# Optimization experiments

Measured on AMD Instinct MI355X. Metric: run time of the kernel, lower is better.

Reference implementation:

```python
import jax, jax.numpy as jnp
import numpy as np

B, N, F_IN, F_OUT, H = 8, 1024, 128, 128, 8
NEG_SLOPE = 0.2


def setup_inputs() -> dict:
    key = jax.random.key(0)
    k1, k2, k3, k4, k5 = jax.random.split(key, 5)
    h = jax.random.normal(k1, (B, N, F_IN), dtype=jnp.float32)
    adj = jax.random.randint(k2, (N, N), 0, 2, dtype=jnp.int32)
    bias_matrix = jax.random.normal(k3, (1, 1, N, N), dtype=jnp.float32)
    # Xavier-uniform-ish parameter init matching torch Parameter shapes
    limW = float(np.sqrt(6.0 / (F_IN + F_OUT)))
    W = jax.random.uniform(k4, (H, F_IN, F_OUT), minval=-limW, maxval=limW, dtype=jnp.float32)
    lima = float(np.sqrt(6.0 / (2 * F_OUT + 1)))
    a = jax.random.uniform(k5, (H, 2 * F_OUT, 1), minval=-lima, maxval=lima, dtype=jnp.float32)
    return {"h": h, "adj": adj, "bias_matrix": bias_matrix, "W": W, "a": a}


def reference(h, adj, bias_matrix, W, a):
    # h: [B,N,Fin], adj: [N,N] int, bias_matrix: [1,1,N,N]
    Fo = W.shape[-1]
    h_prime = jnp.einsum('bni,hio->bnho', h, W)  # [B,N,H,Fo]
    # e[b,i,j,h] = leakyrelu(cat(hp_i, hp_j) . a_h) = leakyrelu(hp_i.a1 + hp_j.a2)
    a1 = a[:, :Fo, 0]   # [H,Fo]
    a2 = a[:, Fo:, 0]   # [H,Fo]
    s_i = jnp.einsum('bnhf,hf->bnh', h_prime, a1)  # [B,N,H]
    s_j = jnp.einsum('bnhf,hf->bnh', h_prime, a2)  # [B,N,H]
    e = jax.nn.leaky_relu(s_i[:, :, None, :] + s_j[:, None, :, :], NEG_SLOPE)  # [B,N,N,H]
    # bias: [1,1,N,N] -> expand(B,1,N,N) -> permute -> [B,N,N,1] -> broadcast H
    e = e + bias_matrix[0, 0][None, :, :, None]
    mask = (adj != 0)[None, :, :, None]  # [1,N,N,1]
    e = jnp.where(mask, e, -jnp.inf)
    attention = jax.nn.softmax(e, axis=2)  # softmax over source nodes j
    h_out = jnp.einsum('bijh,bjhf->bihf', attention, h_prime)  # [B,N,H,Fo]
    # concat=False -> mean over heads
    return h_out.mean(axis=2)  # [B,N,Fo]
```

## Files before the change

kernel.cpp:

```cpp
#include <hip/hip_runtime.h>
#include <hip/hip_bf16.h>
#include <math.h>

#define B_   8
#define N_   1024
#define FIN  128
#define FOUT 128
#define H_   8
#define NEG  0.2f
#define LOG2E 1.4426950408889634f

typedef __attribute__((ext_vector_type(4))) float f32x4;
typedef __attribute__((ext_vector_type(8))) short s16x8;

static __device__ __forceinline__ unsigned short f2bf(float f) {
    unsigned int u = __float_as_uint(f);
    unsigned int r = (u + 0x7fffu + ((u >> 16) & 1u)) >> 16;
    return (unsigned short)r;
}

static __device__ __forceinline__ unsigned short f2bf_hw(float f) {
    union { __hip_bfloat16 b; unsigned short u; } cv;
    cv.b = __float2bfloat16(f);
    return cv.u;
}

__global__ __launch_bounds__(256) void k_prep(const int* __restrict__ adj,
                                              const float* __restrict__ bias,
                                              const float* __restrict__ W,
                                              const float* __restrict__ a,
                                              const float* __restrict__ hsrc,
                                              float* __restrict__ biasm,
                                              unsigned short* __restrict__ WT,
                                              float* __restrict__ wa,
                                              unsigned short* __restrict__ hbT,
                                              float* __restrict__ outz) {
    __shared__ float tf[64][132];
    const int blk = blockIdx.x;
    const int t   = threadIdx.x;

    if (blk < 1024) {
        const int base = (blk * 256 + t) * 4;
        int4   av = *(const int4*)&adj[base];
        float4 bv = *(const float4*)&bias[base];
        const float NINF = -__builtin_inff();
        float4 r;
        r.x = av.x ? bv.x * LOG2E : NINF;
        r.y = av.y ? bv.y * LOG2E : NINF;
        r.z = av.z ? bv.z * LOG2E : NINF;
        r.w = av.w ? bv.w * LOG2E : NINF;
        *(float4*)&biasm[base] = r;
    } else if (blk < 1032) {
        const int hd  = blk - 1024;
        const int fo  = t >> 1;
        const int fi0 = (t & 1) * 64;
        const float* src = W + (size_t)hd * FIN * FOUT;
        unsigned short* dst = WT + ((size_t)hd * FOUT + fo) * FIN + fi0;
#pragma unroll
        for (int c = 0; c < 8; ++c) {
            s16x8 v;
#pragma unroll
            for (int u = 0; u < 8; ++u)
                v[u] = (short)f2bf(src[(size_t)(fi0 + c * 8 + u) * FOUT + fo]);
            *(s16x8*)(dst + c * 8) = v;
        }
    } else if (blk < 1040) {
        const int hd = blk - 1032;
        const int which = t >> 7, k = t & 127;
        const float* wrow = W + ((size_t)hd * FIN + k) * FOUT;
        const float* av   = a + (size_t)hd * 2 * FOUT + which * FOUT;
        float s = 0.f;
#pragma unroll 8
        for (int f = 0; f < FOUT; f += 4) {
            float4 wv = *(const float4*)&wrow[f];
            float4 a4 = *(const float4*)&av[f];
            s += wv.x * a4.x + wv.y * a4.y + wv.z * a4.z + wv.w * a4.w;
        }
        wa[((size_t)hd * 2 + which) * FIN + k] = s * LOG2E;
    } else if (blk < 1168) {
        const int bn0 = (blk - 1040) * 64;
        const int b   = bn0 >> 10;
        const int n0  = bn0 & 1023;
        {
            const int r = t >> 2, k0 = (t & 3) * 32;
            const float* src = hsrc + (size_t)(bn0 + r) * FIN + k0;
#pragma unroll
            for (int c = 0; c < 8; ++c)
                *(float4*)&tf[r][k0 + c * 4] = *(const float4*)&src[c * 4];
        }
        __syncthreads();
        {
            const int k   = t >> 1;
            const int seg = (t & 1) * 32;
            unsigned short* dst = hbT + ((size_t)b * FIN + k) * N_ + n0 + seg;
#pragma unroll
            for (int c = 0; c < 4; ++c) {
                s16x8 v;
#pragma unroll
                for (int u = 0; u < 8; ++u)
                    v[u] = (short)f2bf_hw(tf[seg + c * 8 + u][k]);
                *(s16x8*)(dst + c * 8) = v;
            }
        }
    } else {
        const int base = ((blk - 1168) * 256 + t) * 8;
        const float4 z4 = make_float4(0.f, 0.f, 0.f, 0.f);
        *(float4*)&outz[base]     = z4;
        *(float4*)&outz[base + 4] = z4;
    }
}

__global__ __launch_bounds__(256) void k_s12(const float* __restrict__ hsrc,
                                             const float* __restrict__ wa,
                                             float* __restrict__ s1,
                                             float* __restrict__ s2T) {
    __shared__ float hrow[16][132];
    __shared__ float wal[16][132];
    const int t   = threadIdx.x;
    const int bn0 = blockIdx.x * 16;
    {
        const int r = t >> 4, c = (t & 15) * 8;
        *(float4*)&wal[r][c]     = *(const float4*)&wa[r * FIN + c];
        *(float4*)&wal[r][c + 4] = *(const float4*)&wa[r * FIN + c + 4];
        *(float4*)&hrow[r][c]     = *(const float4*)&hsrc[(size_t)(bn0 + r) * FIN + c];
        *(float4*)&hrow[r][c + 4] = *(const float4*)&hsrc[(size_t)(bn0 + r) * FIN + c + 4];
    }
    __syncthreads();
    const int r = t >> 4, sub = t & 15;
    const int hd = sub >> 1, which = sub & 1;
    float s = 0.f;
#pragma unroll 8
    for (int k = 0; k < FIN; k += 4) {
        float4 hv = *(const float4*)&hrow[r][k];
        float4 wv = *(const float4*)&wal[sub][k];
        s += hv.x * wv.x + hv.y * wv.y + hv.z * wv.z + hv.w * wv.w;
    }
    const int bn = bn0 + r;
    if (which == 0) s1[(size_t)bn * 8 + hd] = s;
    else            s2T[(size_t)hd * (B_ * N_) + bn] = s;
}

__global__ __launch_bounds__(256, 5) void k_pv2(const unsigned short* __restrict__ hbT,
                                                const float* __restrict__ s1,
                                                const float* __restrict__ s2T,
                                                const float* __restrict__ biasm,
                                                const unsigned short* __restrict__ WT,
                                                float* __restrict__ out) {
    __shared__ __align__(16) unsigned short P[32][72];
    __shared__ __align__(16) unsigned short Bl[128 * 64];
    __shared__ __align__(16) unsigned short Gl[32][136];
    __shared__ float Zl[32];
    const int t    = threadIdx.x;
    const int lane = t & 63;
    const int wave = t >> 6;
    const int wg  = blockIdx.x;
    const int swz = ((wg & 7) << 8) | (wg >> 3);
    const int i0  = (swz & 31) * 32;
    const int hd  = (swz >> 5) & 7;
    const int b   = swz >> 8;

    const int prow = t >> 3;
    const int pj0  = (t & 7) * 8;
    const int gi   = (b << 10) + i0 + prow;
    const float s1v = s1[(size_t)gi * 8 + hd];
    const float* bm_row = biasm + (size_t)(i0 + prow) * N_;
    const float* s2p    = s2T + (size_t)hd * (B_ * N_) + (b << 10);

    const unsigned short* hpS = hbT + (size_t)b * FIN * N_;
    const int brow = t >> 3;
    const int bc   = t & 7;

    const int wr = (wave & 1) * 16;
    const int wc = (wave >> 1) * 64;
    const int arow = wr + (lane & 15);
    const int koff = (lane >> 4) * 8;

    f32x4 acc[4];
#pragma unroll
    for (int j = 0; j < 4; ++j) acc[j] = (f32x4){0.f, 0.f, 0.f, 0.f};
    float z_acc = 0.f;

    float4 bmv[2], sv[2];
    s16x8 Breg[4];

    auto load_it = [&](int j0) {
#pragma unroll
        for (int q = 0; q < 2; ++q) {
            bmv[q] = *(const float4*)&bm_row[j0 + pj0 + q * 4];
            sv[q]  = *(const float4*)&s2p[j0 + pj0 + q * 4];
        }
    };
    auto bload = [&](int j0) {
#pragma unroll
        for (int q = 0; q < 4; ++q)
            Breg[q] = *(const s16x8*)&hpS[(size_t)(brow + q * 32) * N_ + j0 + bc * 8];
    };
    auto phaseA = [&]() {
#pragma unroll
        for (int q = 0; q < 4; ++q) {
            int row = brow + q * 32;
            *(s16x8*)&Bl[row * 64 + ((bc ^ (row & 7)) * 8)] = Breg[q];
        }
        s16x8 pv;
#pragma unroll
        for (int q = 0; q < 2; ++q) {
            float x0 = s1v + sv[q].x; x0 = fmaxf(x0, NEG * x0) + bmv[q].x;
            float x1 = s1v + sv[q].y; x1 = fmaxf(x1, NEG * x1) + bmv[q].y;
            float x2 = s1v + sv[q].z; x2 = fmaxf(x2, NEG * x2) + bmv[q].z;
            float x3 = s1v + sv[q].w; x3 = fmaxf(x3, NEG * x3) + bmv[q].w;
            float p0 = exp2f(x0);
            float p1 = exp2f(x1);
            float p2 = exp2f(x2);
            float p3 = exp2f(x3);
            z_acc += (p0 + p1) + (p2 + p3);
            pv[q * 4 + 0] = (short)f2bf_hw(p0);
            pv[q * 4 + 1] = (short)f2bf_hw(p1);
            pv[q * 4 + 2] = (short)f2bf_hw(p2);
            pv[q * 4 + 3] = (short)f2bf_hw(p3);
        }
        *(s16x8*)&P[prow][pj0] = pv;
    };

    bload(0);
    load_it(0);
    for (int it = 0; it < 16; ++it) {
        const int j0 = it * 64;
        phaseA();
        __syncthreads();
        if (it < 15) { bload(j0 + 64); load_it(j0 + 64); }
#pragma unroll
        for (int kw = 0; kw < 2; ++kw) {
            s16x8 a0 = *(const s16x8*)&P[arow][kw * 32 + koff];
#pragma unroll
            for (int fc = 0; fc < 4; ++fc) {
                const int r = wc + fc * 16 + (lane & 15);
                const int chunk = (lane >> 4) + kw * 4;
                s16x8 bf = *(const s16x8*)&Bl[r * 64 + ((chunk ^ (r & 7)) * 8)];
                acc[fc] = __builtin_amdgcn_mfma_f32_16x16x32_bf16(a0, bf, acc[fc], 0, 0, 0);
            }
        }
        __syncthreads();
    }

    float z = z_acc;
    z += __shfl_xor(z, 1); z += __shfl_xor(z, 2); z += __shfl_xor(z, 4);
    if ((t & 7) == 0) Zl[prow] = 0.125f / z;

    const unsigned short* Wsrc = WT + (size_t)hd * FOUT * FIN;
    s16x8 Wreg[4];
#pragma unroll
    for (int q = 0; q < 4; ++q)
        Wreg[q] = *(const s16x8*)&Wsrc[(size_t)(brow + q * 32) * FIN + bc * 8];
    __syncthreads();

#pragma unroll
    for (int r = 0; r < 4; ++r) {
        const int il = wr + (lane >> 4) * 4 + r;
        const float sc = Zl[il];
#pragma unroll
        for (int fc = 0; fc < 4; ++fc)
            Gl[il][wc + fc * 16 + (lane & 15)] = f2bf_hw(acc[fc][r] * sc);
    }
#pragma unroll
    for (int q = 0; q < 4; ++q) {
        int row = brow + q * 32;
        *(s16x8*)&Bl[row * 64 + ((bc ^ (row & 7)) * 8)] = Wreg[q];
    }
#pragma unroll
    for (int q = 0; q < 4; ++q)
        Wreg[q] = *(const s16x8*)&Wsrc[(size_t)(brow + q * 32) * FIN + 64 + bc * 8];
    __syncthreads();

    const int wr2 = (wave & 1) * 16;
    const int wc2 = (wave >> 1) * 64;
    f32x4 acc2[4];
#pragma unroll
    for (int j = 0; j < 4; ++j) acc2[j] = (f32x4){0.f, 0.f, 0.f, 0.f};

#pragma unroll
    for (int kw = 0; kw < 2; ++kw) {
        s16x8 a0 = *(const s16x8*)&Gl[wr2 + (lane & 15)][kw * 32 + koff];
#pragma unroll
        for (int fc = 0; fc < 4; ++fc) {
            const int rb = wc2 + fc * 16 + (lane & 15);
            const int chunk = (lane >> 4) + kw * 4;
            s16x8 bf = *(const s16x8*)&Bl[rb * 64 + ((chunk ^ (rb & 7)) * 8)];
            acc2[fc] = __builtin_amdgcn_mfma_f32_16x16x32_bf16(a0, bf, acc2[fc], 0, 0, 0);
        }
    }
    __syncthreads();
#pragma unroll
    for (int q = 0; q < 4; ++q) {
        int row = brow + q * 32;
        *(s16x8*)&Bl[row * 64 + ((bc ^ (row & 7)) * 8)] = Wreg[q];
    }
    __syncthreads();
#pragma unroll
    for (int kw = 0; kw < 2; ++kw) {
        s16x8 a0 = *(const s16x8*)&Gl[wr2 + (lane & 15)][64 + kw * 32 + koff];
#pragma unroll
        for (int fc = 0; fc < 4; ++fc) {
            const int rb = wc2 + fc * 16 + (lane & 15);
            const int chunk = (lane >> 4) + kw * 4;
            s16x8 bf = *(const s16x8*)&Bl[rb * 64 + ((chunk ^ (rb & 7)) * 8)];
            acc2[fc] = __builtin_amdgcn_mfma_f32_16x16x32_bf16(a0, bf, acc2[fc], 0, 0, 0);
        }
    }

#pragma unroll
    for (int r = 0; r < 4; ++r) {
        const int il = wr2 + (lane >> 4) * 4 + r;
        float* op = out + ((size_t)((b << 10) + i0 + il)) * FOUT + wc2 + (lane & 15);
#pragma unroll
        for (int fc = 0; fc < 4; ++fc)
            unsafeAtomicAdd(op + fc * 16, acc2[fc][r]);
    }
}

extern "C" void kernel_launch(void* const* d_in, const int* in_sizes, int n_in,
                              void* d_out, int out_size, void* d_ws, size_t ws_size,
                              hipStream_t stream) {
    const float* hsrc = (const float*)d_in[0];
    const int*   adj  = (const int*)d_in[1];
    const float* bias = (const float*)d_in[2];
    const float* W    = (const float*)d_in[3];
    const float* a    = (const float*)d_in[4];
    float* out = (float*)d_out;

    char* ws = (char*)d_ws;
    unsigned short* hbT = (unsigned short*)ws;
    float* s1    = (float*)(ws + 2097152);
    float* s2T   = s1 + 65536;
    float* biasm = s2T + 65536;
    unsigned short* WT = (unsigned short*)(biasm + N_ * N_);
    float* wa = (float*)(WT + (size_t)H_ * FOUT * FIN);

    k_prep<<<dim3(1680), 256, 0, stream>>>(adj, bias, W, a, hsrc,
                                           biasm, WT, wa, hbT, out);
    k_s12<<<dim3(B_ * N_ / 16), 256, 0, stream>>>(hsrc, wa, s1, s2T);
    k_pv2<<<dim3(2048), 256, 0, stream>>>(hbT, s1, s2T, biasm, WT, out);
}
```

Before: 76.29 us.

## Process two heads per workgroup to reuse staged h tiles, swizzle P, move zeroing

Each k_pv2 workgroup now handles two attention heads, so the bf16 h tile staged in shared memory is loaded once and feeds two sets of MFMAs. This halves the grid and halves the global traffic for h and the bias matrix. The P buffer is doubled and gets an XOR swizzle to avoid LDS bank conflicts, and output zeroing moves from k_prep into k_s12. The cost is more accumulator registers, so the occupancy hint drops from 5 to 4, and the per-block epilogue does twice the W projection work serially.

```diff
diff --git a/kernel.cpp b/kernel.cpp
--- a/kernel.cpp
+++ b/kernel.cpp
@@ -33,8 +33,7 @@
                                               float* __restrict__ biasm,
                                               unsigned short* __restrict__ WT,
                                               float* __restrict__ wa,
-                                              unsigned short* __restrict__ hbT,
-                                              float* __restrict__ outz) {
+                                              unsigned short* __restrict__ hbT) {
     __shared__ float tf[64][132];
     const int blk = blockIdx.x;
     const int t   = threadIdx.x;
@@ -77,7 +76,7 @@
             s += wv.x * a4.x + wv.y * a4.y + wv.z * a4.z + wv.w * a4.w;
         }
         wa[((size_t)hd * 2 + which) * FIN + k] = s * LOG2E;
-    } else if (blk < 1168) {
+    } else {
         const int bn0 = (blk - 1040) * 64;
         const int b   = bn0 >> 10;
         const int n0  = bn0 & 1023;
@@ -102,22 +101,26 @@
                 *(s16x8*)(dst + c * 8) = v;
             }
         }
-    } else {
-        const int base = ((blk - 1168) * 256 + t) * 8;
+    }
+}
+
+__global__ __launch_bounds__(256) void k_s12(const float* __restrict__ hsrc,
+                                             const float* __restrict__ wa,
+                                             float* __restrict__ s1,
+                                             float* __restrict__ s2T,
+                                             float* __restrict__ outz) {
+    __shared__ float hrow[16][132];
+    __shared__ float wal[16][132];
+    const int t   = threadIdx.x;
+    const int blk = blockIdx.x;
+    if (blk >= 512) {
+        const int base = ((blk - 512) * 256 + t) * 8;
         const float4 z4 = make_float4(0.f, 0.f, 0.f, 0.f);
         *(float4*)&outz[base]     = z4;
         *(float4*)&outz[base + 4] = z4;
-    }
-}
-
-__global__ __launch_bounds__(256) void k_s12(const float* __restrict__ hsrc,
-                                             const float* __restrict__ wa,
-                                             float* __restrict__ s1,
-                                             float* __restrict__ s2T) {
-    __shared__ float hrow[16][132];
-    __shared__ float wal[16][132];
-    const int t   = threadIdx.x;
-    const int bn0 = blockIdx.x * 16;
+        return;
+    }
+    const int bn0 = blk * 16;
     {
         const int r = t >> 4, c = (t & 15) * 8;
         *(float4*)&wal[r][c]     = *(const float4*)&wa[r * FIN + c];
@@ -140,31 +143,35 @@
     else            s2T[(size_t)hd * (B_ * N_) + bn] = s;
 }
 
-__global__ __launch_bounds__(256, 5) void k_pv2(const unsigned short* __restrict__ hbT,
+__global__ __launch_bounds__(256, 4) void k_pv2(const unsigned short* __restrict__ hbT,
                                                 const float* __restrict__ s1,
                                                 const float* __restrict__ s2T,
                                                 const float* __restrict__ biasm,
                                                 const unsigned short* __restrict__ WT,
                                                 float* __restrict__ out) {
-    __shared__ __align__(16) unsigned short P[32][72];
+    __shared__ __align__(16) unsigned short P[2][32 * 64];
     __shared__ __align__(16) unsigned short Bl[128 * 64];
     __shared__ __align__(16) unsigned short Gl[32][136];
-    __shared__ float Zl[32];
+    __shared__ float Zl[2][32];
     const int t    = threadIdx.x;
     const int lane = t & 63;
     const int wave = t >> 6;
     const int wg  = blockIdx.x;
-    const int swz = ((wg & 7) << 8) | (wg >> 3);
+    const int swz = ((wg & 7) << 7) | (wg >> 3);
     const int i0  = (swz & 31) * 32;
-    const int hd  = (swz >> 5) & 7;
-    const int b   = swz >> 8;
+    const int hp  = (swz >> 5) & 3;
+    const int b   = swz >> 7;
+    const int hd0 = hp * 2, hd1 = hd0 + 1;
 
     const int prow = t >> 3;
     const int pj0  = (t & 7) * 8;
+    const int pchk = (t & 7) ^ (prow & 7);
     const int gi   = (b << 10) + i0 + prow;
-    const float s1v = s1[(size_t)gi * 8 + hd];
+    const float s1v0 = s1[(size_t)gi * 8 + hd0];
+    const float s1v1 = s1[(size_t)gi * 8 + hd1];
     const float* bm_row = biasm + (size_t)(i0 + prow) * N_;
-    const float* s2p    = s2T + (size_t)hd * (B_ * N_) + (b << 10);
+    const float* s2p0   = s2T + (size_t)hd0 * (B_ * N_) + (b << 10);
+    const float* s2p1   = s2T + (size_t)hd1 * (B_ * N_) + (b << 10);
 
     const unsigned short* hpS = hbT + (size_t)b * FIN * N_;
     const int brow = t >> 3;
@@ -175,19 +182,23 @@
     const int arow = wr + (lane & 15);
     const int koff = (lane >> 4) * 8;
 
-    f32x4 acc[4];
-#pragma unroll
-    for (int j = 0; j < 4; ++j) acc[j] = (f32x4){0.f, 0.f, 0.f, 0.f};
-    float z_acc = 0.f;
-
-    float4 bmv[2], sv[2];
+    f32x4 acc0[4], acc1[4];
+#pragma unroll
+    for (int j = 0; j < 4; ++j) {
+        acc0[j] = (f32x4){0.f, 0.f, 0.f, 0.f};
+        acc1[j] = (f32x4){0.f, 0.f, 0.f, 0.f};
+    }
+    float z0 = 0.f, z1 = 0.f;
+
+    float4 bmv[2], sv0[2], sv1[2];
     s16x8 Breg[4];
 
     auto load_it = [&](int j0) {
 #pragma unroll
         for (int q = 0; q < 2; ++q) {
             bmv[q] = *(const float4*)&bm_row[j0 + pj0 + q * 4];
-            sv[q]  = *(const float4*)&s2p[j0 + pj0 + q * 4];
+            sv0[q] = *(const float4*)&s2p0[j0 + pj0 + q * 4];
+            sv1[q] = *(const float4*)&s2p1[j0 + pj0 + q * 4];
         }
     };
     auto bload = [&](int j0) {
@@ -195,30 +206,34 @@
         for (int q = 0; q < 4; ++q)
             Breg[q] = *(const s16x8*)&hpS[(size_t)(brow + q * 32) * N_ + j0 + bc * 8];
     };
-    auto phaseA = [&]() {
-#pragma unroll
-        for (int q = 0; q < 4; ++q) {
-            int row = brow + q * 32;
-            *(s16x8*)&Bl[row * 64 + ((bc ^ (row & 7)) * 8)] = Breg[q];
-        }
+    auto pgen = [&](int h, float s1v, const float4* svh, float& zr) {
         s16x8 pv;
 #pragma unroll
         for (int q = 0; q < 2; ++q) {
-            float x0 = s1v + sv[q].x; x0 = fmaxf(x0, NEG * x0) + bmv[q].x;
-            float x1 = s1v + sv[q].y; x1 = fmaxf(x1, NEG * x1) + bmv[q].y;
-            float x2 = s1v + sv[q].z; x2 = fmaxf(x2, NEG * x2) + bmv[q].z;
-            float x3 = s1v + sv[q].w; x3 = fmaxf(x3, NEG * x3) + bmv[q].w;
+            float x0 = s1v + svh[q].x; x0 = fmaxf(x0, NEG * x0) + bmv[q].x;
+            float x1 = s1v + svh[q].y; x1 = fmaxf(x1, NEG * x1) + bmv[q].y;
+            float x2 = s1v + svh[q].z; x2 = fmaxf(x2, NEG * x2) + bmv[q].z;
+            float x3 = s1v + svh[q].w; x3 = fmaxf(x3, NEG * x3) + bmv[q].w;
             float p0 = exp2f(x0);
             float p1 = exp2f(x1);
             float p2 = exp2f(x2);
             float p3 = exp2f(x3);
-            z_acc += (p0 + p1) + (p2 + p3);
+            zr += (p0 + p1) + (p2 + p3);
             pv[q * 4 + 0] = (short)f2bf_hw(p0);
             pv[q * 4 + 1] = (short)f2bf_hw(p1);
             pv[q * 4 + 2] = (short)f2bf_hw(p2);
             pv[q * 4 + 3] = (short)f2bf_hw(p3);
         }
-        *(s16x8*)&P[prow][pj0] = pv;
+        *(s16x8*)&P[h][prow * 64 + pchk * 8] = pv;
+    };
+    auto phaseA = [&]() {
+#pragma unroll
+        for (int q = 0; q < 4; ++q) {
+            int row = brow + q * 32;
+            *(s16x8*)&Bl[row * 64 + ((bc ^ (row & 7)) * 8)] = Breg[q];
+        }
+        pgen(0, s1v0, sv0, z0);
+        pgen(1, s1v1, sv1, z1);
     };
 
     bload(0);
@@ -230,45 +245,37 @@
         if (it < 15) { bload(j0 + 64); load_it(j0 + 64); }
 #pragma unroll
         for (int kw = 0; kw < 2; ++kw) {
-            s16x8 a0 = *(const s16x8*)&P[arow][kw * 32 + koff];
+            const int chunk = kw * 4 + (lane >> 4);
+            const int aoff = (chunk ^ (arow & 7)) * 8;
+            s16x8 a00 = *(const s16x8*)&P[0][arow * 64 + aoff];
+            s16x8 a01 = *(const s16x8*)&P[1][arow * 64 + aoff];
 #pragma unroll
             for (int fc = 0; fc < 4; ++fc) {
                 const int r = wc + fc * 16 + (lane & 15);
-                const int chunk = (lane >> 4) + kw * 4;
                 s16x8 bf = *(const s16x8*)&Bl[r * 64 + ((chunk ^ (r & 7)) * 8)];
-                acc[fc] = __builtin_amdgcn_mfma_f32_16x16x32_bf16(a0, bf, acc[fc], 0, 0, 0);
+                acc0[fc] = __builtin_amdgcn_mfma_f32_16x16x32_bf16(a00, bf, acc0[fc], 0, 0, 0);
+                acc1[fc] = __builtin_amdgcn_mfma_f32_16x16x32_bf16(a01, bf, acc1[fc], 0, 0, 0);
             }
         }
         __syncthreads();
     }
 
-    float z = z_acc;
-    z += __shfl_xor(z, 1); z += __shfl_xor(z, 2); z += __shfl_xor(z, 4);
-    if ((t & 7) == 0) Zl[prow] = 0.125f / z;
-
-    const unsigned short* Wsrc = WT + (size_t)hd * FOUT * FIN;
+    {
+        float za = z0, zb = z1;
+        za += __shfl_xor(za, 1); za += __shfl_xor(za, 2); za += __shfl_xor(za, 4);
+        zb += __shfl_xor(zb, 1); zb += __shfl_xor(zb, 2); zb += __shfl_xor(zb, 4);
+        if ((t & 7) == 0) {
+            Zl[0][prow] = 0.125f / za;
+            Zl[1][prow] = 0.125f / zb;
+        }
+    }
+
+    const unsigned short* Wsrc0 = WT + (size_t)hd0 * FOUT * FIN;
+    const unsigned short* Wsrc1 = WT + (size_t)hd1 * FOUT * FIN;
     s16x8 Wreg[4];
 #pragma unroll
     for (int q = 0; q < 4; ++q)
-        Wreg[q] = *(const s16x8*)&Wsrc[(size_t)(brow + q * 32) * FIN + bc * 8];
-    __syncthreads();
-
-#pragma unroll
-    for (int r = 0; r < 4; ++r) {
-        const int il = wr + (lane >> 4) * 4 + r;
-        const float sc = Zl[il];
-#pragma unroll
-        for (int fc = 0; fc < 4; ++fc)
-            Gl[il][wc + fc * 16 + (lane & 15)] = f2bf_hw(acc[fc][r] * sc);
-    }
-#pragma unroll
-    for (int q = 0; q < 4; ++q) {
-        int row = brow + q * 32;
-        *(s16x8*)&Bl[row * 64 + ((bc ^ (row & 7)) * 8)] = Wreg[q];
-    }
-#pragma unroll
-    for (int q = 0; q < 4; ++q)
-        Wreg[q] = *(const s16x8*)&Wsrc[(size_t)(brow + q * 32) * FIN + 64 + bc * 8];
+        Wreg[q] = *(const s16x8*)&Wsrc0[(size_t)(brow + q * 32) * FIN + bc * 8];
     __syncthreads();
 
     const int wr2 = (wave & 1) * 16;
@@ -277,35 +284,68 @@
 #pragma unroll
     for (int j = 0; j < 4; ++j) acc2[j] = (f32x4){0.f, 0.f, 0.f, 0.f};
 
-#pragma unroll
-    for (int kw = 0; kw < 2; ++kw) {
-        s16x8 a0 = *(const s16x8*)&Gl[wr2 + (lane & 15)][kw * 32 + koff];
-#pragma unroll
-        for (int fc = 0; fc < 4; ++fc) {
-            const int rb = wc2 + fc * 16 + (lane & 15);
-            const int chunk = (lane >> 4) + kw * 4;
-            s16x8 bf = *(const s16x8*)&Bl[rb * 64 + ((chunk ^ (rb & 7)) * 8)];
-            acc2[fc] = __builtin_amdgcn_mfma_f32_16x16x32_bf16(a0, bf, acc2[fc], 0, 0, 0);
-        }
-    }
-    __syncthreads();
-#pragma unroll
-    for (int q = 0; q < 4; ++q) {
-        int row = brow + q * 32;
-        *(s16x8*)&Bl[row * 64 + ((bc ^ (row & 7)) * 8)] = Wreg[q];
-    }
-    __syncthreads();
-#pragma unroll
-    for (int kw = 0; kw < 2; ++kw) {
-        s16x8 a0 = *(const s16x8*)&Gl[wr2 + (lane & 15)][64 + kw * 32 + koff];
-#pragma unroll
-        for (int fc = 0; fc < 4; ++fc) {
-            const int rb = wc2 + fc * 16 + (lane & 15);
-            const int chunk = (lane >> 4) + kw * 4;
-            s16x8 bf = *(const s16x8*)&Bl[rb * 64 + ((chunk ^ (rb & 7)) * 8)];
-            acc2[fc] = __builtin_amdgcn_mfma_f32_16x16x32_bf16(a0, bf, acc2[fc], 0, 0, 0);
-        }
-    }
+    auto wstage = [&]() {
+#pragma unroll
+        for (int q = 0; q < 4; ++q) {
+            int row = brow + q * 32;
+            *(s16x8*)&Bl[row * 64 + ((bc ^ (row & 7)) * 8)] = Wreg[q];
+        }
+    };
+    auto gw_mfma = [&](int half) {
+#pragma unroll
+        for (int kw = 0; kw < 2; ++kw) {
+            const int chunk = kw * 4 + (lane >> 4);
+            s16x8 a0 = *(const s16x8*)&Gl[wr2 + (lane & 15)][half * 64 + kw * 32 + koff];
+#pragma unroll
+            for (int fc = 0; fc < 4; ++fc) {
+                const int rb = wc2 + fc * 16 + (lane & 15);
+                s16x8 bf = *(const s16x8*)&Bl[rb * 64 + ((chunk ^ (rb & 7)) * 8)];
+                acc2[fc] = __builtin_amdgcn_mfma_f32_16x16x32_bf16(a0, bf, acc2[fc], 0, 0, 0);
+            }
+        }
+    };
+
+#pragma unroll
+    for (int r = 0; r < 4; ++r) {
+        const int il = wr + (lane >> 4) * 4 + r;
+        const float sc = Zl[0][il];
+#pragma unroll
+        for (int fc = 0; fc < 4; ++fc)
+            Gl[il][wc + fc * 16 + (lane & 15)] = f2bf_hw(acc0[fc][r] * sc);
+    }
+    wstage();
+#pragma unroll
+    for (int q = 0; q < 4; ++q)
+        Wreg[q] = *(const s16x8*)&Wsrc0[(size_t)(brow + q * 32) * FIN + 64 + bc * 8];
+    __syncthreads();
+    gw_mfma(0);
+    __syncthreads();
+    wstage();
+#pragma unroll
+    for (int q = 0; q < 4; ++q)
+        Wreg[q] = *(const s16x8*)&Wsrc1[(size_t)(brow + q * 32) * FIN + bc * 8];
+    __syncthreads();
+    gw_mfma(1);
+    __syncthreads();
+
+#pragma unroll
+    for (int r = 0; r < 4; ++r) {
+        const int il = wr + (lane >> 4) * 4 + r;
+        const float sc = Zl[1][il];
+#pragma unroll
+        for (int fc = 0; fc < 4; ++fc)
+            Gl[il][wc + fc * 16 + (lane & 15)] = f2bf_hw(acc1[fc][r] * sc);
+    }
+    wstage();
+#pragma unroll
+    for (int q = 0; q < 4; ++q)
+        Wreg[q] = *(const s16x8*)&Wsrc1[(size_t)(brow + q * 32) * FIN + 64 + bc * 8];
+    __syncthreads();
+    gw_mfma(0);
+    __syncthreads();
+    wstage();
+    __syncthreads();
+    gw_mfma(1);
 
 #pragma unroll
     for (int r = 0; r < 4; ++r) {
@@ -335,8 +375,8 @@
     unsigned short* WT = (unsigned short*)(biasm + N_ * N_);
     float* wa = (float*)(WT + (size_t)H_ * FOUT * FIN);
 
-    k_prep<<<dim3(1680), 256, 0, stream>>>(adj, bias, W, a, hsrc,
-                                           biasm, WT, wa, hbT, out);
-    k_s12<<<dim3(B_ * N_ / 16), 256, 0, stream>>>(hsrc, wa, s1, s2T);
-    k_pv2<<<dim3(2048), 256, 0, stream>>>(hbT, s1, s2T, biasm, WT, out);
-}
+    k_prep<<<dim3(1168), 256, 0, stream>>>(adj, bias, W, a, hsrc,
+                                           biasm, WT, wa, hbT);
+    k_s12<<<dim3(1024), 256, 0, stream>>>(hsrc, wa, s1, s2T, out);
+    k_pv2<<<dim3(1024), 256, 0, stream>>>(hbT, s1, s2T, biasm, WT, out);
+}
```

Measured after the change: 63.38 us (median of 2 runs). -16.9%, faster.

## Process four heads per workgroup sharing h tiles, fold score kernel into prep

Applied to the files above, without the earlier changes.

The attention kernel now handles four heads per workgroup, so each loaded tile of transposed h is reused across four heads' P@V MFMAs instead of one. The grid shrinks from 2048 to 512 blocks and register use grows, with launch bounds relaxed to 2 waves per SIMD. The output projection loops over the four heads, accumulating into a single tile before the atomic add. The separate s1/s2 score kernel is merged into the prep kernel, removing one launch and the wa round trip. The risk is lower occupancy and fewer blocks, which may underfill the GPU.

```diff
diff --git a/kernel.cpp b/kernel.cpp
--- a/kernel.cpp
+++ b/kernel.cpp
@@ -32,10 +32,12 @@
                                               const float* __restrict__ hsrc,
                                               float* __restrict__ biasm,
                                               unsigned short* __restrict__ WT,
-                                              float* __restrict__ wa,
+                                              float* __restrict__ s1,
+                                              float* __restrict__ s2T,
                                               unsigned short* __restrict__ hbT,
                                               float* __restrict__ outz) {
     __shared__ float tf[64][132];
+    __shared__ float wal[2][128];
     const int blk = blockIdx.x;
     const int t   = threadIdx.x;
 
@@ -64,21 +66,8 @@
                 v[u] = (short)f2bf(src[(size_t)(fi0 + c * 8 + u) * FOUT + fo]);
             *(s16x8*)(dst + c * 8) = v;
         }
-    } else if (blk < 1040) {
-        const int hd = blk - 1032;
-        const int which = t >> 7, k = t & 127;
-        const float* wrow = W + ((size_t)hd * FIN + k) * FOUT;
-        const float* av   = a + (size_t)hd * 2 * FOUT + which * FOUT;
-        float s = 0.f;
-#pragma unroll 8
-        for (int f = 0; f < FOUT; f += 4) {
-            float4 wv = *(const float4*)&wrow[f];
-            float4 a4 = *(const float4*)&av[f];
-            s += wv.x * a4.x + wv.y * a4.y + wv.z * a4.z + wv.w * a4.w;
-        }
-        wa[((size_t)hd * 2 + which) * FIN + k] = s * LOG2E;
-    } else if (blk < 1168) {
-        const int bn0 = (blk - 1040) * 64;
+    } else if (blk < 1160) {
+        const int bn0 = (blk - 1032) * 64;
         const int b   = bn0 >> 10;
         const int n0  = bn0 & 1023;
         {
@@ -102,69 +91,84 @@
                 *(s16x8*)(dst + c * 8) = v;
             }
         }
+    } else if (blk < 1224) {
+        const int q  = blk - 1160;
+        const int b  = q >> 3, hd = q & 7;
+        {
+            const int which = t >> 7, k = t & 127;
+            const float* wrow = W + ((size_t)hd * FIN + k) * FOUT;
+            const float* av   = a + (size_t)hd * 2 * FOUT + which * FOUT;
+            float s = 0.f;
+#pragma unroll 8
+            for (int f = 0; f < FOUT; f += 4) {
+                float4 wv = *(const float4*)&wrow[f];
+                float4 a4 = *(const float4*)&av[f];
+                s += wv.x * a4.x + wv.y * a4.y + wv.z * a4.z + wv.w * a4.w;
+            }
+            wal[which][k] = s * LOG2E;
+        }
+        __syncthreads();
+        const int rg = t >> 3;
+        const int f0 = (t & 7) * 16;
+        for (int c = 0; c < 32; ++c) {
+            const int n = c * 32 + rg;
+            const float* hr = hsrc + ((size_t)(b << 10) + n) * FIN + f0;
+            float s1p = 0.f, s2p = 0.f;
+#pragma unroll
+            for (int u = 0; u < 4; ++u) {
+                float4 hv = *(const float4*)&hr[u * 4];
+                float4 w1 = *(const float4*)&wal[0][f0 + u * 4];
+                float4 w2 = *(const float4*)&wal[1][f0 + u * 4];
+                s1p += hv.x * w1.x + hv.y * w1.y + hv.z * w1.z + hv.w * w1.w;
+                s2p += hv.x * w2.x + hv.y * w2.y + hv.z * w2.z + hv.w * w2.w;
+            }
+            s1p += __shfl_xor(s1p, 1); s1p += __shfl_xor(s1p, 2); s1p += __shfl_xor(s1p, 4);
+            s2p += __shfl_xor(s2p, 1); s2p += __shfl_xor(s2p, 2); s2p += __shfl_xor(s2p, 4);
+            if ((t & 7) == 0) {
+                s1[((size_t)(b << 10) + n) * 8 + hd] = s1p;
+                s2T[(size_t)hd * (B_ * N_) + (b << 10) + n] = s2p;
+            }
+        }
     } else {
-        const int base = ((blk - 1168) * 256 + t) * 8;
+        const int base = ((blk - 1224) * 256 + t) * 8;
         const float4 z4 = make_float4(0.f, 0.f, 0.f, 0.f);
         *(float4*)&outz[base]     = z4;
         *(float4*)&outz[base + 4] = z4;
     }
 }
 
-__global__ __launch_bounds__(256) void k_s12(const float* __restrict__ hsrc,
-                                             const float* __restrict__ wa,
-                                             float* __restrict__ s1,
-                                             float* __restrict__ s2T) {
-    __shared__ float hrow[16][132];
-    __shared__ float wal[16][132];
-    const int t   = threadIdx.x;
-    const int bn0 = blockIdx.x * 16;
-    {
-        const int r = t >> 4, c = (t & 15) * 8;
-        *(float4*)&wal[r][c]     = *(const float4*)&wa[r * FIN + c];
-        *(float4*)&wal[r][c + 4] = *(const float4*)&wa[r * FIN + c + 4];
-        *(float4*)&hrow[r][c]     = *(const float4*)&hsrc[(size_t)(bn0 + r) * FIN + c];
-        *(float4*)&hrow[r][c + 4] = *(const float4*)&hsrc[(size_t)(bn0 + r) * FIN + c + 4];
-    }
-    __syncthreads();
-    const int r = t >> 4, sub = t & 15;
-    const int hd = sub >> 1, which = sub & 1;
-    float s = 0.f;
-#pragma unroll 8
-    for (int k = 0; k < FIN; k += 4) {
-        float4 hv = *(const float4*)&hrow[r][k];
-        float4 wv = *(const float4*)&wal[sub][k];
-        s += hv.x * wv.x + hv.y * wv.y + hv.z * wv.z + hv.w * wv.w;
-    }
-    const int bn = bn0 + r;
-    if (which == 0) s1[(size_t)bn * 8 + hd] = s;
-    else            s2T[(size_t)hd * (B_ * N_) + bn] = s;
-}
-
-__global__ __launch_bounds__(256, 5) void k_pv2(const unsigned short* __restrict__ hbT,
+__global__ __launch_bounds__(256, 2) void k_pv2(const unsigned short* __restrict__ hbT,
                                                 const float* __restrict__ s1,
                                                 const float* __restrict__ s2T,
                                                 const float* __restrict__ biasm,
                                                 const unsigned short* __restrict__ WT,
                                                 float* __restrict__ out) {
-    __shared__ __align__(16) unsigned short P[32][72];
+    __shared__ __align__(16) unsigned short Pm[4 * 2048];
     __shared__ __align__(16) unsigned short Bl[128 * 64];
     __shared__ __align__(16) unsigned short Gl[32][136];
-    __shared__ float Zl[32];
+    __shared__ float Zl[4][32];
     const int t    = threadIdx.x;
     const int lane = t & 63;
     const int wave = t >> 6;
     const int wg  = blockIdx.x;
-    const int swz = ((wg & 7) << 8) | (wg >> 3);
+    const int swz = ((wg & 7) << 6) | (wg >> 3);
     const int i0  = (swz & 31) * 32;
-    const int hd  = (swz >> 5) & 7;
-    const int b   = swz >> 8;
+    const int hg  = (swz >> 5) & 1;
+    const int b   = swz >> 6;
+    const int hd0 = hg * 4;
 
     const int prow = t >> 3;
     const int pj0  = (t & 7) * 8;
+    const int pchk = (t & 7) ^ (prow & 7);
     const int gi   = (b << 10) + i0 + prow;
-    const float s1v = s1[(size_t)gi * 8 + hd];
+    float s1v[4];
+#pragma unroll
+    for (int h = 0; h < 4; ++h) s1v[h] = s1[(size_t)gi * 8 + hd0 + h];
     const float* bm_row = biasm + (size_t)(i0 + prow) * N_;
-    const float* s2p    = s2T + (size_t)hd * (B_ * N_) + (b << 10);
+    const float* s2p[4];
+#pragma unroll
+    for (int h = 0; h < 4; ++h)
+        s2p[h] = s2T + (size_t)(hd0 + h) * (B_ * N_) + (b << 10);
 
     const unsigned short* hpS = hbT + (size_t)b * FIN * N_;
     const int brow = t >> 3;
@@ -175,20 +179,25 @@
     const int arow = wr + (lane & 15);
     const int koff = (lane >> 4) * 8;
 
-    f32x4 acc[4];
-#pragma unroll
-    for (int j = 0; j < 4; ++j) acc[j] = (f32x4){0.f, 0.f, 0.f, 0.f};
-    float z_acc = 0.f;
-
-    float4 bmv[2], sv[2];
+    f32x4 acc[4][4];
+#pragma unroll
+    for (int h = 0; h < 4; ++h)
+#pragma unroll
+        for (int j = 0; j < 4; ++j) acc[h][j] = (f32x4){0.f, 0.f, 0.f, 0.f};
+    float zh[4] = {0.f, 0.f, 0.f, 0.f};
+
+    float4 bmv[2], sv[4][2];
     s16x8 Breg[4];
 
     auto load_it = [&](int j0) {
 #pragma unroll
-        for (int q = 0; q < 2; ++q) {
+        for (int q = 0; q < 2; ++q)
             bmv[q] = *(const float4*)&bm_row[j0 + pj0 + q * 4];
-            sv[q]  = *(const float4*)&s2p[j0 + pj0 + q * 4];
-        }
+#pragma unroll
+        for (int h = 0; h < 4; ++h)
+#pragma unroll
+            for (int q = 0; q < 2; ++q)
+                sv[h][q] = *(const float4*)&s2p[h][j0 + pj0 + q * 4];
     };
     auto bload = [&](int j0) {
 #pragma unroll
@@ -201,24 +210,27 @@
             int row = brow + q * 32;
             *(s16x8*)&Bl[row * 64 + ((bc ^ (row & 7)) * 8)] = Breg[q];
         }
-        s16x8 pv;
-#pragma unroll
-        for (int q = 0; q < 2; ++q) {
-            float x0 = s1v + sv[q].x; x0 = fmaxf(x0, NEG * x0) + bmv[q].x;
-            float x1 = s1v + sv[q].y; x1 = fmaxf(x1, NEG * x1) + bmv[q].y;
-            float x2 = s1v + sv[q].z; x2 = fmaxf(x2, NEG * x2) + bmv[q].z;
-            float x3 = s1v + sv[q].w; x3 = fmaxf(x3, NEG * x3) + bmv[q].w;
-            float p0 = exp2f(x0);
-            float p1 = exp2f(x1);
-            float p2 = exp2f(x2);
-            float p3 = exp2f(x3);
-            z_acc += (p0 + p1) + (p2 + p3);
-            pv[q * 4 + 0] = (short)f2bf_hw(p0);
-            pv[q * 4 + 1] = (short)f2bf_hw(p1);
-            pv[q * 4 + 2] = (short)f2bf_hw(p2);
-            pv[q * 4 + 3] = (short)f2bf_hw(p3);
-        }
-        *(s16x8*)&P[prow][pj0] = pv;
+#pragma unroll
+        for (int h = 0; h < 4; ++h) {
+            s16x8 pv;
+#pragma unroll
+            for (int q = 0; q < 2; ++q) {
+                float x0 = s1v[h] + sv[h][q].x; x0 = fmaxf(x0, NEG * x0) + bmv[q].x;
+                float x1 = s1v[h] + sv[h][q].y; x1 = fmaxf(x1, NEG * x1) + bmv[q].y;
+                float x2 = s1v[h] + sv[h][q].z; x2 = fmaxf(x2, NEG * x2) + bmv[q].z;
+                float x3 = s1v[h] + sv[h][q].w; x3 = fmaxf(x3, NEG * x3) + bmv[q].w;
+                float p0 = exp2f(x0);
+                float p1 = exp2f(x1);
+                float p2 = exp2f(x2);
+                float p3 = exp2f(x3);
+                zh[h] += (p0 + p1) + (p2 + p3);
+                pv[q * 4 + 0] = (short)f2bf_hw(p0);
+                pv[q * 4 + 1] = (short)f2bf_hw(p1);
+                pv[q * 4 + 2] = (short)f2bf_hw(p2);
+                pv[q * 4 + 3] = (short)f2bf_hw(p3);
+            }
+            *(s16x8*)&Pm[h * 2048 + prow * 64 + pchk * 8] = pv;
+        }
     };
 
     bload(0);
@@ -230,81 +242,97 @@
         if (it < 15) { bload(j0 + 64); load_it(j0 + 64); }
 #pragma unroll
         for (int kw = 0; kw < 2; ++kw) {
-            s16x8 a0 = *(const s16x8*)&P[arow][kw * 32 + koff];
+            const int chunk = kw * 4 + (lane >> 4);
+            const int aoff = arow * 64 + ((chunk ^ (arow & 7)) * 8);
+            s16x8 a0 = *(const s16x8*)&Pm[aoff];
+            s16x8 a1 = *(const s16x8*)&Pm[2048 + aoff];
+            s16x8 a2 = *(const s16x8*)&Pm[4096 + aoff];
+            s16x8 a3 = *(const s16x8*)&Pm[6144 + aoff];
 #pragma unroll
             for (int fc = 0; fc < 4; ++fc) {
                 const int r = wc + fc * 16 + (lane & 15);
-                const int chunk = (lane >> 4) + kw * 4;
                 s16x8 bf = *(const s16x8*)&Bl[r * 64 + ((chunk ^ (r & 7)) * 8)];
-                acc[fc] = __builtin_amdgcn_mfma_f32_16x16x32_bf16(a0, bf, acc[fc], 0, 0, 0);
-            }
-        }
-        __syncthreads();
-    }
-
-    float z = z_acc;
-    z += __shfl_xor(z, 1); z += __shfl_xor(z, 2); z += __shfl_xor(z, 4);
-    if ((t & 7) == 0) Zl[prow] = 0.125f / z;
-
-    const unsigned short* Wsrc = WT + (size_t)hd * FOUT * FIN;
-    s16x8 Wreg[4];
-#pragma unroll
-    for (int q = 0; q < 4; ++q)
-        Wreg[q] = *(const s16x8*)&Wsrc[(size_t)(brow + q * 32) * FIN + bc * 8];
+                acc[0][fc] = __builtin_amdgcn_mfma_f32_16x16x32_bf16(a0, bf, acc[0][fc], 0, 0, 0);
+                acc[1][fc] = __builtin_amdgcn_mfma_f32_16x16x32_bf16(a1, bf, acc[1][fc], 0, 0, 0);
+                acc[2][fc] = __builtin_amdgcn_mfma_f32_16x16x32_bf16(a2, bf, acc[2][fc], 0, 0, 0);
+                acc[3][fc] = __builtin_amdgcn_mfma_f32_16x16x32_bf16(a3, bf, acc[3][fc], 0, 0, 0);
+            }
+        }
+        __syncthreads();
+    }
+
+#pragma unroll
+    for (int h = 0; h < 4; ++h) {
+        float z = zh[h];
+        z += __shfl_xor(z, 1); z += __shfl_xor(z, 2); z += __shfl_xor(z, 4);
+        if ((t & 7) == 0) Zl[h][prow] = 0.125f / z;
+    }
+
+    unsigned short* Pf = &Pm[0];
+    const int wr2 = wr, wc2 = wc;
+    f32x4 acc2[4];
+#pragma unroll
+    for (int j = 0; j < 4; ++j) acc2[j] = (f32x4){0.f, 0.f, 0.f, 0.f};
+
+    s16x8 WregA[4], WregB[4];
+    {
+        const unsigned short* Ws = WT + (size_t)hd0 * FOUT * FIN;
+#pragma unroll
+        for (int q = 0; q < 4; ++q) {
+            WregA[q] = *(const s16x8*)&Ws[(size_t)(brow + q * 32) * FIN + bc * 8];
+            WregB[q] = *(const s16x8*)&Ws[(size_t)(brow + q * 32) * FIN + 64 + bc * 8];
+        }
+    }
     __syncthreads();
 
 #pragma unroll
-    for (int r = 0; r < 4; ++r) {
-        const int il = wr + (lane >> 4) * 4 + r;
-        const float sc = Zl[il];
-#pragma unroll
-        for (int fc = 0; fc < 4; ++fc)
-            Gl[il][wc + fc * 16 + (lane & 15)] = f2bf_hw(acc[fc][r] * sc);
-    }
-#pragma unroll
-    for (int q = 0; q < 4; ++q) {
-        int row = brow + q * 32;
-        *(s16x8*)&Bl[row * 64 + ((bc ^ (row & 7)) * 8)] = Wreg[q];
-    }
-#pragma unroll
-    for (int q = 0; q < 4; ++q)
-        Wreg[q] = *(const s16x8*)&Wsrc[(size_t)(brow + q * 32) * FIN + 64 + bc * 8];
-    __syncthreads();
-
-    const int wr2 = (wave & 1) * 16;
-    const int wc2 = (wave >> 1) * 64;
-    f32x4 acc2[4];
-#pragma unroll
-    for (int j = 0; j < 4; ++j) acc2[j] = (f32x4){0.f, 0.f, 0.f, 0.f};
-
-#pragma unroll
-    for (int kw = 0; kw < 2; ++kw) {
-        s16x8 a0 = *(const s16x8*)&Gl[wr2 + (lane & 15)][kw * 32 + koff];
-#pragma unroll
-        for (int fc = 0; fc < 4; ++fc) {
-            const int rb = wc2 + fc * 16 + (lane & 15);
-            const int chunk = (lane >> 4) + kw * 4;
-            s16x8 bf = *(const s16x8*)&Bl[rb * 64 + ((chunk ^ (rb & 7)) * 8)];
-            acc2[fc] = __builtin_amdgcn_mfma_f32_16x16x32_bf16(a0, bf, acc2[fc], 0, 0, 0);
-        }
-    }
-    __syncthreads();
-#pragma unroll
-    for (int q = 0; q < 4; ++q) {
-        int row = brow + q * 32;
-        *(s16x8*)&Bl[row * 64 + ((bc ^ (row & 7)) * 8)] = Wreg[q];
-    }
-    __syncthreads();
-#pragma unroll
-    for (int kw = 0; kw < 2; ++kw) {
-        s16x8 a0 = *(const s16x8*)&Gl[wr2 + (lane & 15)][64 + kw * 32 + koff];
-#pragma unroll
-        for (int fc = 0; fc < 4; ++fc) {
-            const int rb = wc2 + fc * 16 + (lane & 15);
-            const int chunk = (lane >> 4) + kw * 4;
-            s16x8 bf = *(const s16x8*)&Bl[rb * 64 + ((chunk ^ (rb & 7)) * 8)];
-            acc2[fc] = __builtin_amdgcn_mfma_f32_16x16x32_bf16(a0, bf, acc2[fc], 0, 0, 0);
-        }
+    for (int h = 0; h < 4; ++h) {
+#pragma unroll
+        for (int r = 0; r < 4; ++r) {
+            const int il = wr + (lane >> 4) * 4 + r;
+            const float sc = Zl[h][il];
+#pragma unroll
+            for (int fc = 0; fc < 4; ++fc)
+                Gl[il][wc + fc * 16 + (lane & 15)] = f2bf_hw(acc[h][fc][r] * sc);
+        }
+#pragma unroll
+        for (int q = 0; q < 4; ++q) {
+            int row = brow + q * 32;
+            *(s16x8*)&Bl[row * 64 + ((bc ^ (row & 7)) * 8)] = WregA[q];
+            *(s16x8*)&Pf[row * 64 + ((bc ^ (row & 7)) * 8)] = WregB[q];
+        }
+        if (h < 3) {
+            const unsigned short* Ws = WT + (size_t)(hd0 + h + 1) * FOUT * FIN;
+#pragma unroll
+            for (int q = 0; q < 4; ++q) {
+                WregA[q] = *(const s16x8*)&Ws[(size_t)(brow + q * 32) * FIN + bc * 8];
+                WregB[q] = *(const s16x8*)&Ws[(size_t)(brow + q * 32) * FIN + 64 + bc * 8];
+            }
+        }
+        __syncthreads();
+#pragma unroll
+        for (int kw = 0; kw < 2; ++kw) {
+            const int chunk = kw * 4 + (lane >> 4);
+            s16x8 a0 = *(const s16x8*)&Gl[wr2 + (lane & 15)][kw * 32 + koff];
+#pragma unroll
+            for (int fc = 0; fc < 4; ++fc) {
+                const int rb = wc2 + fc * 16 + (lane & 15);
+                s16x8 bf = *(const s16x8*)&Bl[rb * 64 + ((chunk ^ (rb & 7)) * 8)];
+                acc2[fc] = __builtin_amdgcn_mfma_f32_16x16x32_bf16(a0, bf, acc2[fc], 0, 0, 0);
+            }
+        }
+#pragma unroll
+        for (int kw = 0; kw < 2; ++kw) {
+            const int chunk = kw * 4 + (lane >> 4);
+            s16x8 a0 = *(const s16x8*)&Gl[wr2 + (lane & 15)][64 + kw * 32 + koff];
+#pragma unroll
+            for (int fc = 0; fc < 4; ++fc) {
+                const int rb = wc2 + fc * 16 + (lane & 15);
+                s16x8 bf = *(const s16x8*)&Pf[rb * 64 + ((chunk ^ (rb & 7)) * 8)];
+                acc2[fc] = __builtin_amdgcn_mfma_f32_16x16x32_bf16(a0, bf, acc2[fc], 0, 0, 0);
+            }
+        }
+        __syncthreads();
     }
 
 #pragma unroll
@@ -333,10 +361,8 @@
     float* s2T   = s1 + 65536;
     float* biasm = s2T + 65536;
     unsigned short* WT = (unsigned short*)(biasm + N_ * N_);
-    float* wa = (float*)(WT + (size_t)H_ * FOUT * FIN);
-
-    k_prep<<<dim3(1680), 256, 0, stream>>>(adj, bias, W, a, hsrc,
-                                           biasm, WT, wa, hbT, out);
-    k_s12<<<dim3(B_ * N_ / 16), 256, 0, stream>>>(hsrc, wa, s1, s2T);
-    k_pv2<<<dim3(2048), 256, 0, stream>>>(hbT, s1, s2T, biasm, WT, out);
-}
+
+    k_prep<<<dim3(1736), 256, 0, stream>>>(adj, bias, W, a, hsrc,
+                                           biasm, WT, s1, s2T, hbT, out);
+    k_pv2<<<dim3(512), 256, 0, stream>>>(hbT, s1, s2T, biasm, WT, out);
+}
```

Measured after the change: 79.93 us. +4.8%, slower.
